# Kernel optimization log

Hardware: AMD Instinct MI355X
Metric: run time of the kernel (lower is better)

Reference implementation:

```python
import jax, jax.numpy as jnp
import numpy as np

IN_CHANNELS = 128
NUM_OUTPUTS = 4
BATCH_SIZE = 4096
N_NODES = 500000


def setup_inputs() -> dict:
    key = jax.random.key(0)
    ks = jax.random.split(key, 8)
    C = IN_CHANNELS
    k = jax.random.normal(ks[0], (N_NODES, C), dtype=jnp.float32)
    v = jax.random.normal(ks[1], (N_NODES, C), dtype=jnp.float32)
    h = jax.random.normal(ks[2], (BATCH_SIZE * C,), dtype=jnp.float32)
    batch = jnp.sort(jax.random.randint(ks[3], (N_NODES,), 0, BATCH_SIZE)).astype(jnp.int64)
    s = 1.0 / np.sqrt(C)
    # torch LSTM params: input size 2C, hidden C, gate order (i, f, g, o)
    W_ih = jax.random.uniform(ks[4], (4 * C, 2 * C), minval=-s, maxval=s, dtype=jnp.float32)
    W_hh = jax.random.uniform(ks[5], (4 * C, C), minval=-s, maxval=s, dtype=jnp.float32)
    b_ih = jax.random.uniform(ks[6], (4 * C,), minval=-s, maxval=s, dtype=jnp.float32)
    b_hh = jax.random.uniform(ks[7], (4 * C,), minval=-s, maxval=s, dtype=jnp.float32)
    return {"k": k, "v": v, "h": h, "W_ih": W_ih, "W_hh": W_hh,
            "b_ih": b_ih, "b_hh": b_hh, "batch": batch}


def _lstm_cell(x, h0, c0, W_ih, W_hh, b_ih, b_hh):
    C = h0.shape[-1]
    gates = x @ W_ih.T + b_ih + h0 @ W_hh.T + b_hh  # [B, 4C]
    i, f, g, o = jnp.split(gates, 4, axis=-1)
    c = jax.nn.sigmoid(f) * c0 + jax.nn.sigmoid(i) * jnp.tanh(g)
    h = jax.nn.sigmoid(o) * jnp.tanh(c)
    return h, c


def reference(k, v, h, W_ih, W_hh, b_ih, b_hh, batch):
    C = k.shape[-1]
    B = h.shape[0] // C  # num_layers=1
    batch = batch.astype(jnp.int32)
    h0 = h.reshape(B, C)
    c0 = h.reshape(B, C)
    q_star = jnp.zeros((B, 2 * C), dtype=v.dtype)
    readouts = []
    for _ in range(NUM_OUTPUTS):
        h0, c0 = _lstm_cell(q_star, h0, c0, W_ih, W_hh, b_ih, b_hh)
        q = h0  # [B, C]
        e = jnp.sum(k * q[batch], axis=-1)  # [N]
        m = jax.ops.segment_max(e, batch, num_segments=B, indices_are_sorted=True)
        ex = jnp.exp(e - m[batch])
        s = jax.ops.segment_sum(ex, batch, num_segments=B, indices_are_sorted=True)
        a = ex / (s[batch] + 1e-16)  # segment softmax
        r = jax.ops.segment_sum(a[:, None] * v, batch, num_segments=B, indices_are_sorted=True)  # [B, C]
        readouts.append(r)
        q_star = jnp.concatenate([q, r], axis=-1)
    return jnp.concatenate(readouts, axis=-1)  # [B, C*NUM_OUTPUTS]
```

## Files before the change

### kernel.cpp

```cpp
#include <hip/hip_runtime.h>
#include <math.h>

#define C 128
#define B 4096
#define NNODES 500000
#define NOUT 4
#define KTOT 384


__global__ void init_state(const float* __restrict__ h, float* __restrict__ h0,
                           float* __restrict__ c0, float* __restrict__ q_star,
                           int* __restrict__ seg_start, int* __restrict__ seg_end) {
    int idx = blockIdx.x * blockDim.x + threadIdx.x;
    if (idx < B * 2 * C) q_star[idx] = 0.f;
    if (idx < B * C) { float t = h[idx]; h0[idx] = t; c0[idx] = t; }
    if (idx < B)     { seg_start[idx] = 0; seg_end[idx] = 0; }
}

__global__ void seg_bounds(const int* __restrict__ batch, int* __restrict__ seg_start,
                           int* __restrict__ seg_end) {
    int n = blockIdx.x * blockDim.x + threadIdx.x;
    if (n >= NNODES) return;
    int b = batch[n];
    if (n == 0 || batch[n - 1] != b) seg_start[b] = n;
    if (n == NNODES - 1 || batch[n + 1] != b) seg_end[b] = n + 1;
}

#define BM 64
#define BN 64
#define BK 16
#define LDP 68

__global__ __launch_bounds__(256) void lstm_gemm(
    const float* __restrict__ q_star, const float* __restrict__ h0,
    const float* __restrict__ W_ih, const float* __restrict__ W_hh,
    const float* __restrict__ b_ih, const float* __restrict__ b_hh,
    float* __restrict__ gates) {
    __shared__ float As[BK][LDP];
    __shared__ float Bs[BK][LDP];

    const int bm0 = blockIdx.x * BM;
    const int jn0 = blockIdx.y * BN;
    const int tid = threadIdx.x;
    const int tx = tid & 15;
    const int ty = tid >> 4;

    const int st_row = tid >> 2;
    const int st_k   = (tid & 3) << 2;

    float acc[4][4] = {{0.f}};

    for (int k0 = 0; k0 < KTOT; k0 += BK) {
        float4 av, bv;
        {
            const int gb = bm0 + st_row;
            if (k0 < 256)
                av = *(const float4*)(q_star + (size_t)gb * 256 + (k0 + st_k));
            else
                av = *(const float4*)(h0 + (size_t)gb * 128 + (k0 - 256 + st_k));
            const int gj = jn0 + st_row;
            if (k0 < 256)
                bv = *(const float4*)(W_ih + (size_t)gj * 256 + (k0 + st_k));
            else
                bv = *(const float4*)(W_hh + (size_t)gj * 128 + (k0 - 256 + st_k));
        }
        __syncthreads();
        As[st_k + 0][st_row] = av.x;
        As[st_k + 1][st_row] = av.y;
        As[st_k + 2][st_row] = av.z;
        As[st_k + 3][st_row] = av.w;
        Bs[st_k + 0][st_row] = bv.x;
        Bs[st_k + 1][st_row] = bv.y;
        Bs[st_k + 2][st_row] = bv.z;
        Bs[st_k + 3][st_row] = bv.w;
        __syncthreads();

#pragma unroll
        for (int kk = 0; kk < BK; ++kk) {
            const float4 a4 = *(const float4*)&As[kk][ty << 2];
            const float4 b4 = *(const float4*)&Bs[kk][tx << 2];
            const float a[4] = {a4.x, a4.y, a4.z, a4.w};
            const float bb[4] = {b4.x, b4.y, b4.z, b4.w};
#pragma unroll
            for (int i = 0; i < 4; ++i)
#pragma unroll
                for (int j = 0; j < 4; ++j)
                    acc[i][j] = fmaf(a[i], bb[j], acc[i][j]);
        }
    }

    const int jj = jn0 + (tx << 2);
    const float4 bi = *(const float4*)(b_ih + jj);
    const float4 bh = *(const float4*)(b_hh + jj);
    const float bias[4] = {bi.x + bh.x, bi.y + bh.y, bi.z + bh.z, bi.w + bh.w};
#pragma unroll
    for (int i = 0; i < 4; ++i) {
        const int gb = bm0 + (ty << 2) + i;
        float4 o;
        o.x = acc[i][0] + bias[0];
        o.y = acc[i][1] + bias[1];
        o.z = acc[i][2] + bias[2];
        o.w = acc[i][3] + bias[3];
        *(float4*)(gates + (size_t)gb * (4 * C) + jj) = o;
    }
}

__global__ void lstm_act(const float* __restrict__ gates, float* __restrict__ c0,
                         float* __restrict__ h0, float* __restrict__ q_star) {
    int idx = blockIdx.x * blockDim.x + threadIdx.x;
    if (idx >= B * C) return;
    int b = idx / C, c = idx % C;
    const float* g = gates + (size_t)b * 4 * C;
    float ii = g[c];
    float ff = g[C + c];
    float gg = g[2 * C + c];
    float oo = g[3 * C + c];
    float si = 1.f / (1.f + __expf(-ii));
    float sf = 1.f / (1.f + __expf(-ff));
    float so = 1.f / (1.f + __expf(-oo));
    float tg = tanhf(gg);
    float cn = sf * c0[idx] + si * tg;
    float hn = so * tanhf(cn);
    c0[idx] = cn;
    h0[idx] = hn;
    q_star[(size_t)b * 2 * C + c] = hn;
}

__global__ __launch_bounds__(256) void attention(
    const float* __restrict__ k, const float* __restrict__ v,
    const float* __restrict__ h0, const int* __restrict__ seg_start,
    const int* __restrict__ seg_end, float* __restrict__ e_ws,
    float* __restrict__ q_star, float* __restrict__ out, int t) {
    const int b = blockIdx.x;
    const int tid = threadIdx.x;
    const int w = tid >> 6;
    const int lane = tid & 63;
    const int g = lane >> 4;
    const int j = lane & 15;
    const int ch = j << 3;

    __shared__ float red[4];
    __shared__ float racc[16][C];

    const int s0 = seg_start[b];
    const int s1 = seg_end[b];

    const float4 qa = *(const float4*)(h0 + (size_t)b * C + ch);
    const float4 qb = *(const float4*)(h0 + (size_t)b * C + ch + 4);

    float m = -INFINITY;
    for (int n0 = s0 + w * 4; n0 < s1; n0 += 16) {
        const int n = n0 + g;
        if (n < s1) {
            const float4 ka = *(const float4*)(k + (size_t)n * C + ch);
            const float4 kb = *(const float4*)(k + (size_t)n * C + ch + 4);
            float part = ka.x * qa.x + ka.y * qa.y + ka.z * qa.z + ka.w * qa.w
                       + kb.x * qb.x + kb.y * qb.y + kb.z * qb.z + kb.w * qb.w;
            part += __shfl_xor(part, 1);
            part += __shfl_xor(part, 2);
            part += __shfl_xor(part, 4);
            part += __shfl_xor(part, 8);
            if (j == 0) e_ws[n] = part;
            m = fmaxf(m, part);
        }
    }
    m = fmaxf(m, __shfl_xor(m, 16));
    m = fmaxf(m, __shfl_xor(m, 32));
    if (lane == 0) red[w] = m;
    __syncthreads();
    const float M = fmaxf(fmaxf(red[0], red[1]), fmaxf(red[2], red[3]));
    __syncthreads();

    float s = 0.f;
    for (int n = s0 + tid; n < s1; n += 256) s += __expf(e_ws[n] - M);
#pragma unroll
    for (int off = 32; off >= 1; off >>= 1) s += __shfl_xor(s, off);
    if (lane == 0) red[w] = s;
    __syncthreads();
    const float S = red[0] + red[1] + red[2] + red[3];
    const float inv = 1.f / (S + 1e-16f);

    float4 A0 = {0.f, 0.f, 0.f, 0.f}, A1 = {0.f, 0.f, 0.f, 0.f};
    for (int n0 = s0 + w * 4; n0 < s1; n0 += 16) {
        const int n = n0 + g;
        if (n < s1) {
            const float p = __expf(e_ws[n] - M) * inv;
            const float4 va = *(const float4*)(v + (size_t)n * C + ch);
            const float4 vb = *(const float4*)(v + (size_t)n * C + ch + 4);
            A0.x = fmaf(p, va.x, A0.x); A0.y = fmaf(p, va.y, A0.y);
            A0.z = fmaf(p, va.z, A0.z); A0.w = fmaf(p, va.w, A0.w);
            A1.x = fmaf(p, vb.x, A1.x); A1.y = fmaf(p, vb.y, A1.y);
            A1.z = fmaf(p, vb.z, A1.z); A1.w = fmaf(p, vb.w, A1.w);
        }
    }
    *(float4*)&racc[(w << 2) + g][ch]     = A0;
    *(float4*)&racc[(w << 2) + g][ch + 4] = A1;
    __syncthreads();

    if (tid < C) {
        float r = 0.f;
#pragma unroll
        for (int p = 0; p < 16; ++p) r += racc[p][tid];
        out[(size_t)b * (NOUT * C) + t * C + tid] = r;
        q_star[(size_t)b * 2 * C + C + tid] = r;
    }
}

extern "C" void kernel_launch(void* const* d_in, const int* in_sizes, int n_in,
                              void* d_out, int out_size, void* d_ws, size_t ws_size,
                              hipStream_t stream) {
    const float* k    = (const float*)d_in[0];
    const float* v    = (const float*)d_in[1];
    const float* h    = (const float*)d_in[2];
    const float* W_ih = (const float*)d_in[3];
    const float* W_hh = (const float*)d_in[4];
    const float* b_ih = (const float*)d_in[5];
    const float* b_hh = (const float*)d_in[6];
    const int*   batch = (const int*)d_in[7];
    float* out = (float*)d_out;

    float* ws      = (float*)d_ws;
    float* h0      = ws;
    float* c0      = h0 + (size_t)B * C;
    float* q_star  = c0 + (size_t)B * C;
    float* gates   = q_star + (size_t)B * 2 * C;
    float* e_ws    = gates + (size_t)B * 4 * C;
    int*   sstart  = (int*)(e_ws + NNODES);
    int*   send    = sstart + B;

    init_state<<<(B * 2 * C + 255) / 256, 256, 0, stream>>>(h, h0, c0, q_star, sstart, send);
    seg_bounds<<<(NNODES + 255) / 256, 256, 0, stream>>>(batch, sstart, send);

    for (int t = 0; t < NOUT; ++t) {
        lstm_gemm<<<dim3(B / BM, (4 * C) / BN), 256, 0, stream>>>(
            q_star, h0, W_ih, W_hh, b_ih, b_hh, gates);
        lstm_act<<<(B * C + 255) / 256, 256, 0, stream>>>(gates, c0, h0, q_star);
        attention<<<B, 256, 0, stream>>>(k, v, h0, sstart, send, e_ws, q_star, out, t);
    }
}
```

Baseline: 954.9 us.

## Fuse LSTM activation into GEMM, fold weights, single-pass online-softmax attention

Precomputes combined weights (W_ih[:, :C] + W_hh, since the query half of q_star equals h0) with gate-interleaved rows, so one GEMM with K=256 (K=128 at step 0) produces all four gates per channel in a thread and applies the LSTM activation in the epilogue. This removes the gates buffer and the separate activation kernel. Attention becomes a single pass with online softmax that reads k and v together, dropping the e_ws round trip and the second sweep over nodes. The cost is extra exp and rescale work per node and more register pressure, plus a larger 128x64 GEMM tile.

```diff
diff --git a/kernel.cpp b/kernel.cpp
--- a/kernel.cpp
+++ b/kernel.cpp
@@ -5,196 +5,223 @@
 #define B 4096
 #define NNODES 500000
 #define NOUT 4
-#define KTOT 384
-
-
-__global__ void init_state(const float* __restrict__ h, float* __restrict__ h0,
-                           float* __restrict__ c0, float* __restrict__ q_star,
-                           int* __restrict__ seg_start, int* __restrict__ seg_end) {
+
+
+__global__ void init_state(const float* __restrict__ h, float* __restrict__ A0,
+                           float* __restrict__ c0, int* __restrict__ sstart,
+                           int* __restrict__ send) {
     int idx = blockIdx.x * blockDim.x + threadIdx.x;
-    if (idx < B * 2 * C) q_star[idx] = 0.f;
-    if (idx < B * C) { float t = h[idx]; h0[idx] = t; c0[idx] = t; }
-    if (idx < B)     { seg_start[idx] = 0; seg_end[idx] = 0; }
-}
-
-__global__ void seg_bounds(const int* __restrict__ batch, int* __restrict__ seg_start,
-                           int* __restrict__ seg_end) {
+    if (idx < B * 256) {
+        int b = idx >> 8, cc = idx & 255;
+        A0[idx] = (cc < C) ? h[b * C + cc] : 0.f;
+    }
+    if (idx < B * C) c0[idx] = h[idx];
+    if (idx < B) { sstart[idx] = 0; send[idx] = 0; }
+}
+
+__global__ void prep_w(const float* __restrict__ W_ih, const float* __restrict__ W_hh,
+                       const float* __restrict__ b_ih, const float* __restrict__ b_hh,
+                       float* __restrict__ Wc, float* __restrict__ W0,
+                       float* __restrict__ bp) {
+    int idx = blockIdx.x * blockDim.x + threadIdx.x;
+    int n = idx >> 8, kk = idx & 255;
+    int c = n >> 2, gi = n & 3;
+    int j = gi * C + c;
+    float wih = W_ih[(size_t)j * 256 + kk];
+    float val = (kk < C) ? (wih + W_hh[(size_t)j * C + kk]) : wih;
+    Wc[(size_t)n * 256 + kk] = val;
+    if (kk < C) W0[(size_t)n * C + kk] = W_hh[(size_t)j * C + kk];
+    if (kk == 0) bp[n] = b_ih[j] + b_hh[j];
+}
+
+__global__ void seg_bounds(const int* __restrict__ batch, int* __restrict__ sstart,
+                           int* __restrict__ send) {
     int n = blockIdx.x * blockDim.x + threadIdx.x;
     if (n >= NNODES) return;
     int b = batch[n];
-    if (n == 0 || batch[n - 1] != b) seg_start[b] = n;
-    if (n == NNODES - 1 || batch[n + 1] != b) seg_end[b] = n + 1;
-}
-
-#define BM 64
-#define BN 64
-#define BK 16
-#define LDP 68
-
-__global__ __launch_bounds__(256) void lstm_gemm(
-    const float* __restrict__ q_star, const float* __restrict__ h0,
-    const float* __restrict__ W_ih, const float* __restrict__ W_hh,
-    const float* __restrict__ b_ih, const float* __restrict__ b_hh,
-    float* __restrict__ gates) {
-    __shared__ float As[BK][LDP];
-    __shared__ float Bs[BK][LDP];
-
-    const int bm0 = blockIdx.x * BM;
-    const int jn0 = blockIdx.y * BN;
+    if (n == 0 || batch[n - 1] != b) sstart[b] = n;
+    if (n == NNODES - 1 || batch[n + 1] != b) send[b] = n + 1;
+}
+
+#define GBM 128
+#define GBN 64
+#define GBK 16
+
+__global__ __launch_bounds__(256) void lstm_fused(
+    const float* __restrict__ A, const float* __restrict__ W,
+    const float* __restrict__ bp, float* __restrict__ c0,
+    float* __restrict__ Anx, int Klen, int ldw) {
+    __shared__ float As[GBK][132];
+    __shared__ float Bs[GBK][68];
+    const int bm0 = blockIdx.x * GBM;
+    const int jn0 = blockIdx.y * GBN;
     const int tid = threadIdx.x;
-    const int tx = tid & 15;
-    const int ty = tid >> 4;
-
-    const int st_row = tid >> 2;
-    const int st_k   = (tid & 3) << 2;
-
-    float acc[4][4] = {{0.f}};
-
-    for (int k0 = 0; k0 < KTOT; k0 += BK) {
-        float4 av, bv;
-        {
-            const int gb = bm0 + st_row;
-            if (k0 < 256)
-                av = *(const float4*)(q_star + (size_t)gb * 256 + (k0 + st_k));
-            else
-                av = *(const float4*)(h0 + (size_t)gb * 128 + (k0 - 256 + st_k));
-            const int gj = jn0 + st_row;
-            if (k0 < 256)
-                bv = *(const float4*)(W_ih + (size_t)gj * 256 + (k0 + st_k));
-            else
-                bv = *(const float4*)(W_hh + (size_t)gj * 128 + (k0 - 256 + st_k));
+    const int tx = tid & 15, ty = tid >> 4;
+    const int sr = tid >> 2, sk = (tid & 3) << 2;
+
+    float acc[8][4];
+#pragma unroll
+    for (int i = 0; i < 8; ++i)
+#pragma unroll
+        for (int q = 0; q < 4; ++q) acc[i][q] = 0.f;
+
+    for (int k0 = 0; k0 < Klen; k0 += GBK) {
+        const float4 a0 = *(const float4*)(A + (size_t)(bm0 + sr) * 256 + k0 + sk);
+        const float4 a1 = *(const float4*)(A + (size_t)(bm0 + 64 + sr) * 256 + k0 + sk);
+        const float4 bv = *(const float4*)(W + (size_t)(jn0 + sr) * ldw + k0 + sk);
+        __syncthreads();
+        As[sk + 0][sr] = a0.x; As[sk + 1][sr] = a0.y;
+        As[sk + 2][sr] = a0.z; As[sk + 3][sr] = a0.w;
+        As[sk + 0][64 + sr] = a1.x; As[sk + 1][64 + sr] = a1.y;
+        As[sk + 2][64 + sr] = a1.z; As[sk + 3][64 + sr] = a1.w;
+        Bs[sk + 0][sr] = bv.x; Bs[sk + 1][sr] = bv.y;
+        Bs[sk + 2][sr] = bv.z; Bs[sk + 3][sr] = bv.w;
+        __syncthreads();
+#pragma unroll
+        for (int kk = 0; kk < GBK; ++kk) {
+            const float4 af0 = *(const float4*)&As[kk][ty << 3];
+            const float4 af1 = *(const float4*)&As[kk][(ty << 3) + 4];
+            const float4 bf  = *(const float4*)&Bs[kk][tx << 2];
+            const float aa[8] = {af0.x, af0.y, af0.z, af0.w, af1.x, af1.y, af1.z, af1.w};
+            const float bb[4] = {bf.x, bf.y, bf.z, bf.w};
+#pragma unroll
+            for (int i = 0; i < 8; ++i)
+#pragma unroll
+                for (int q = 0; q < 4; ++q)
+                    acc[i][q] = fmaf(aa[i], bb[q], acc[i][q]);
         }
-        __syncthreads();
-        As[st_k + 0][st_row] = av.x;
-        As[st_k + 1][st_row] = av.y;
-        As[st_k + 2][st_row] = av.z;
-        As[st_k + 3][st_row] = av.w;
-        Bs[st_k + 0][st_row] = bv.x;
-        Bs[st_k + 1][st_row] = bv.y;
-        Bs[st_k + 2][st_row] = bv.z;
-        Bs[st_k + 3][st_row] = bv.w;
-        __syncthreads();
-
-#pragma unroll
-        for (int kk = 0; kk < BK; ++kk) {
-            const float4 a4 = *(const float4*)&As[kk][ty << 2];
-            const float4 b4 = *(const float4*)&Bs[kk][tx << 2];
-            const float a[4] = {a4.x, a4.y, a4.z, a4.w};
-            const float bb[4] = {b4.x, b4.y, b4.z, b4.w};
-#pragma unroll
-            for (int i = 0; i < 4; ++i)
-#pragma unroll
-                for (int j = 0; j < 4; ++j)
-                    acc[i][j] = fmaf(a[i], bb[j], acc[i][j]);
-        }
-    }
-
-    const int jj = jn0 + (tx << 2);
-    const float4 bi = *(const float4*)(b_ih + jj);
-    const float4 bh = *(const float4*)(b_hh + jj);
-    const float bias[4] = {bi.x + bh.x, bi.y + bh.y, bi.z + bh.z, bi.w + bh.w};
-#pragma unroll
-    for (int i = 0; i < 4; ++i) {
-        const int gb = bm0 + (ty << 2) + i;
-        float4 o;
-        o.x = acc[i][0] + bias[0];
-        o.y = acc[i][1] + bias[1];
-        o.z = acc[i][2] + bias[2];
-        o.w = acc[i][3] + bias[3];
-        *(float4*)(gates + (size_t)gb * (4 * C) + jj) = o;
-    }
-}
-
-__global__ void lstm_act(const float* __restrict__ gates, float* __restrict__ c0,
-                         float* __restrict__ h0, float* __restrict__ q_star) {
-    int idx = blockIdx.x * blockDim.x + threadIdx.x;
-    if (idx >= B * C) return;
-    int b = idx / C, c = idx % C;
-    const float* g = gates + (size_t)b * 4 * C;
-    float ii = g[c];
-    float ff = g[C + c];
-    float gg = g[2 * C + c];
-    float oo = g[3 * C + c];
-    float si = 1.f / (1.f + __expf(-ii));
-    float sf = 1.f / (1.f + __expf(-ff));
-    float so = 1.f / (1.f + __expf(-oo));
-    float tg = tanhf(gg);
-    float cn = sf * c0[idx] + si * tg;
-    float hn = so * tanhf(cn);
-    c0[idx] = cn;
-    h0[idx] = hn;
-    q_star[(size_t)b * 2 * C + c] = hn;
+    }
+
+    const int c = (jn0 >> 2) + tx;
+    const float4 bb4 = *(const float4*)(bp + jn0 + (tx << 2));
+#pragma unroll
+    for (int i = 0; i < 8; ++i) {
+        const int b = bm0 + (ty << 3) + i;
+        const float gi = acc[i][0] + bb4.x;
+        const float gf = acc[i][1] + bb4.y;
+        const float gg = acc[i][2] + bb4.z;
+        const float go = acc[i][3] + bb4.w;
+        const float si = 1.f / (1.f + __expf(-gi));
+        const float sf = 1.f / (1.f + __expf(-gf));
+        const float so = 1.f / (1.f + __expf(-go));
+        const float tg = tanhf(gg);
+        const float cn = sf * c0[(size_t)b * C + c] + si * tg;
+        const float hn = so * tanhf(cn);
+        c0[(size_t)b * C + c] = cn;
+        Anx[(size_t)b * 256 + c] = hn;
+    }
+}
+
+__device__ __forceinline__ float dot8(const float4 a0, const float4 a1,
+                                      const float4 q0, const float4 q1) {
+    float p = a0.x * q0.x + a0.y * q0.y + a0.z * q0.z + a0.w * q0.w;
+    p += a1.x * q1.x + a1.y * q1.y + a1.z * q1.z + a1.w * q1.w;
+    return p;
 }
 
 __global__ __launch_bounds__(256) void attention(
     const float* __restrict__ k, const float* __restrict__ v,
-    const float* __restrict__ h0, const int* __restrict__ seg_start,
-    const int* __restrict__ seg_end, float* __restrict__ e_ws,
-    float* __restrict__ q_star, float* __restrict__ out, int t) {
+    float* __restrict__ Anx, const int* __restrict__ sstart,
+    const int* __restrict__ send, float* __restrict__ out, int t) {
     const int b = blockIdx.x;
     const int tid = threadIdx.x;
-    const int w = tid >> 6;
-    const int lane = tid & 63;
-    const int g = lane >> 4;
-    const int j = lane & 15;
+    const int w = tid >> 6, lane = tid & 63, g = lane >> 4, j = lane & 15;
     const int ch = j << 3;
 
-    __shared__ float red[4];
+    __shared__ float mred[4], sred[4];
     __shared__ float racc[16][C];
 
-    const int s0 = seg_start[b];
-    const int s1 = seg_end[b];
-
-    const float4 qa = *(const float4*)(h0 + (size_t)b * C + ch);
-    const float4 qb = *(const float4*)(h0 + (size_t)b * C + ch + 4);
-
-    float m = -INFINITY;
-    for (int n0 = s0 + w * 4; n0 < s1; n0 += 16) {
+    const int s0 = sstart[b], s1 = send[b];
+    const int full = (s1 - s0) & ~31;
+    const int sf = s0 + full;
+
+    const float4 qa = *(const float4*)(Anx + (size_t)b * 256 + ch);
+    const float4 qb = *(const float4*)(Anx + (size_t)b * 256 + ch + 4);
+
+    float m = -3.0e38f, s = 0.f;
+    float4 r0 = {0.f, 0.f, 0.f, 0.f}, r1 = {0.f, 0.f, 0.f, 0.f};
+
+    for (int n0 = s0 + (w << 3); n0 < sf; n0 += 32) {
+        const int na = n0 + g, nb = na + 4;
+        const float4 ka0 = *(const float4*)(k + (size_t)na * C + ch);
+        const float4 ka1 = *(const float4*)(k + (size_t)na * C + ch + 4);
+        const float4 kb0 = *(const float4*)(k + (size_t)nb * C + ch);
+        const float4 kb1 = *(const float4*)(k + (size_t)nb * C + ch + 4);
+        const float4 va0 = *(const float4*)(v + (size_t)na * C + ch);
+        const float4 va1 = *(const float4*)(v + (size_t)na * C + ch + 4);
+        const float4 vb0 = *(const float4*)(v + (size_t)nb * C + ch);
+        const float4 vb1 = *(const float4*)(v + (size_t)nb * C + ch + 4);
+        float pa = dot8(ka0, ka1, qa, qb);
+        float pb = dot8(kb0, kb1, qa, qb);
+        pa += __shfl_xor(pa, 1); pb += __shfl_xor(pb, 1);
+        pa += __shfl_xor(pa, 2); pb += __shfl_xor(pb, 2);
+        pa += __shfl_xor(pa, 4); pb += __shfl_xor(pb, 4);
+        pa += __shfl_xor(pa, 8); pb += __shfl_xor(pb, 8);
+        const float mn = fmaxf(m, fmaxf(pa, pb));
+        const float ef = __expf(m - mn);
+        const float wa = __expf(pa - mn);
+        const float wb = __expf(pb - mn);
+        s = s * ef + wa + wb;
+        m = mn;
+        r0.x = fmaf(wb, vb0.x, fmaf(wa, va0.x, r0.x * ef));
+        r0.y = fmaf(wb, vb0.y, fmaf(wa, va0.y, r0.y * ef));
+        r0.z = fmaf(wb, vb0.z, fmaf(wa, va0.z, r0.z * ef));
+        r0.w = fmaf(wb, vb0.w, fmaf(wa, va0.w, r0.w * ef));
+        r1.x = fmaf(wb, vb1.x, fmaf(wa, va1.x, r1.x * ef));
+        r1.y = fmaf(wb, vb1.y, fmaf(wa, va1.y, r1.y * ef));
+        r1.z = fmaf(wb, vb1.z, fmaf(wa, va1.z, r1.z * ef));
+        r1.w = fmaf(wb, vb1.w, fmaf(wa, va1.w, r1.w * ef));
+    }
+    for (int n0 = sf + (w << 2); n0 < s1; n0 += 16) {
         const int n = n0 + g;
         if (n < s1) {
-            const float4 ka = *(const float4*)(k + (size_t)n * C + ch);
-            const float4 kb = *(const float4*)(k + (size_t)n * C + ch + 4);
-            float part = ka.x * qa.x + ka.y * qa.y + ka.z * qa.z + ka.w * qa.w
-                       + kb.x * qb.x + kb.y * qb.y + kb.z * qb.z + kb.w * qb.w;
-            part += __shfl_xor(part, 1);
-            part += __shfl_xor(part, 2);
-            part += __shfl_xor(part, 4);
-            part += __shfl_xor(part, 8);
-            if (j == 0) e_ws[n] = part;
-            m = fmaxf(m, part);
+            const float4 ka0 = *(const float4*)(k + (size_t)n * C + ch);
+            const float4 ka1 = *(const float4*)(k + (size_t)n * C + ch + 4);
+            const float4 va0 = *(const float4*)(v + (size_t)n * C + ch);
+            const float4 va1 = *(const float4*)(v + (size_t)n * C + ch + 4);
+            float p = dot8(ka0, ka1, qa, qb);
+            p += __shfl_xor(p, 1);
+            p += __shfl_xor(p, 2);
+            p += __shfl_xor(p, 4);
+            p += __shfl_xor(p, 8);
+            const float mn = fmaxf(m, p);
+            const float ef = __expf(m - mn);
+            const float wa = __expf(p - mn);
+            s = s * ef + wa;
+            m = mn;
+            r0.x = fmaf(wa, va0.x, r0.x * ef);
+            r0.y = fmaf(wa, va0.y, r0.y * ef);
+            r0.z = fmaf(wa, va0.z, r0.z * ef);
+            r0.w = fmaf(wa, va0.w, r0.w * ef);
+            r1.x = fmaf(wa, va1.x, r1.x * ef);
+            r1.y = fmaf(wa, va1.y, r1.y * ef);
+            r1.z = fmaf(wa, va1.z, r1.z * ef);
+            r1.w = fmaf(wa, va1.w, r1.w * ef);
         }
     }
-    m = fmaxf(m, __shfl_xor(m, 16));
-    m = fmaxf(m, __shfl_xor(m, 32));
-    if (lane == 0) red[w] = m;
+
+    float mw = m, sw = s;
+#pragma unroll
+    for (int off = 16; off <= 32; off <<= 1) {
+        const float om = __shfl_xor(mw, off);
+        const float os = __shfl_xor(sw, off);
+        const float mn = fmaxf(mw, om);
+        sw = sw * __expf(mw - mn) + os * __expf(om - mn);
+        mw = mn;
+    }
+    if (lane == 0) { mred[w] = mw; sred[w] = sw; }
     __syncthreads();
-    const float M = fmaxf(fmaxf(red[0], red[1]), fmaxf(red[2], red[3]));
-    __syncthreads();
-
-    float s = 0.f;
-    for (int n = s0 + tid; n < s1; n += 256) s += __expf(e_ws[n] - M);
-#pragma unroll
-    for (int off = 32; off >= 1; off >>= 1) s += __shfl_xor(s, off);
-    if (lane == 0) red[w] = s;
-    __syncthreads();
-    const float S = red[0] + red[1] + red[2] + red[3];
+    const float M = fmaxf(fmaxf(mred[0], mred[1]), fmaxf(mred[2], mred[3]));
+    const float S = sred[0] * __expf(mred[0] - M) + sred[1] * __expf(mred[1] - M)
+                  + sred[2] * __expf(mred[2] - M) + sred[3] * __expf(mred[3] - M);
     const float inv = 1.f / (S + 1e-16f);
 
-    float4 A0 = {0.f, 0.f, 0.f, 0.f}, A1 = {0.f, 0.f, 0.f, 0.f};
-    for (int n0 = s0 + w * 4; n0 < s1; n0 += 16) {
-        const int n = n0 + g;
-        if (n < s1) {
-            const float p = __expf(e_ws[n] - M) * inv;
-            const float4 va = *(const float4*)(v + (size_t)n * C + ch);
-            const float4 vb = *(const float4*)(v + (size_t)n * C + ch + 4);
-            A0.x = fmaf(p, va.x, A0.x); A0.y = fmaf(p, va.y, A0.y);
-            A0.z = fmaf(p, va.z, A0.z); A0.w = fmaf(p, va.w, A0.w);
-            A1.x = fmaf(p, vb.x, A1.x); A1.y = fmaf(p, vb.y, A1.y);
-            A1.z = fmaf(p, vb.z, A1.z); A1.w = fmaf(p, vb.w, A1.w);
-        }
-    }
-    *(float4*)&racc[(w << 2) + g][ch]     = A0;
-    *(float4*)&racc[(w << 2) + g][ch + 4] = A1;
+    const float sc = __expf(m - M) * inv;
+    float4 w0 = r0, w1 = r1;
+    w0.x *= sc; w0.y *= sc; w0.z *= sc; w0.w *= sc;
+    w1.x *= sc; w1.y *= sc; w1.z *= sc; w1.w *= sc;
+    *(float4*)&racc[(w << 2) + g][ch]     = w0;
+    *(float4*)&racc[(w << 2) + g][ch + 4] = w1;
     __syncthreads();
 
     if (tid < C) {
@@ -202,7 +229,7 @@
 #pragma unroll
         for (int p = 0; p < 16; ++p) r += racc[p][tid];
         out[(size_t)b * (NOUT * C) + t * C + tid] = r;
-        q_star[(size_t)b * 2 * C + C + tid] = r;
+        Anx[(size_t)b * 256 + C + tid] = r;
     }
 }
 
@@ -219,22 +246,30 @@
     const int*   batch = (const int*)d_in[7];
     float* out = (float*)d_out;
 
-    float* ws      = (float*)d_ws;
-    float* h0      = ws;
-    float* c0      = h0 + (size_t)B * C;
-    float* q_star  = c0 + (size_t)B * C;
-    float* gates   = q_star + (size_t)B * 2 * C;
-    float* e_ws    = gates + (size_t)B * 4 * C;
-    int*   sstart  = (int*)(e_ws + NNODES);
-    int*   send    = sstart + B;
-
-    init_state<<<(B * 2 * C + 255) / 256, 256, 0, stream>>>(h, h0, c0, q_star, sstart, send);
+    float* ws  = (float*)d_ws;
+    float* A0v = ws;
+    float* A1v = A0v + (size_t)B * 256;
+    float* c0  = A1v + (size_t)B * 256;
+    float* Wc  = c0 + (size_t)B * C;
+    float* W0  = Wc + 512 * 256;
+    float* bp  = W0 + 512 * C;
+    int* sstart = (int*)(bp + 512);
+    int* send   = sstart + B;
+
+    init_state<<<(B * 256 + 255) / 256, 256, 0, stream>>>(h, A0v, c0, sstart, send);
+    prep_w<<<(512 * 256) / 256, 256, 0, stream>>>(W_ih, W_hh, b_ih, b_hh, Wc, W0, bp);
     seg_bounds<<<(NNODES + 255) / 256, 256, 0, stream>>>(batch, sstart, send);
 
+    float* Abuf[2] = {A0v, A1v};
     for (int t = 0; t < NOUT; ++t) {
-        lstm_gemm<<<dim3(B / BM, (4 * C) / BN), 256, 0, stream>>>(
-            q_star, h0, W_ih, W_hh, b_ih, b_hh, gates);
-        lstm_act<<<(B * C + 255) / 256, 256, 0, stream>>>(gates, c0, h0, q_star);
-        attention<<<B, 256, 0, stream>>>(k, v, h0, sstart, send, e_ws, q_star, out, t);
-    }
-}
+        const float* Acur = Abuf[t & 1];
+        float* Anx = Abuf[(t + 1) & 1];
+        if (t == 0)
+            lstm_fused<<<dim3(B / GBM, 512 / GBN), 256, 0, stream>>>(
+                Acur, W0, bp, c0, Anx, C, C);
+        else
+            lstm_fused<<<dim3(B / GBM, 512 / GBN), 256, 0, stream>>>(
+                Acur, Wc, bp, c0, Anx, 256, 256);
+        attention<<<B, 256, 0, stream>>>(k, v, Anx, sstart, send, out, t);
+    }
+}
```

Result: faster. 917.2 us (-4.0%).
